# Kernel tuning notes

Measured on AMD Instinct MI355X. Metric: run time of the kernel, lower is better.

## Reference

```python
import jax, jax.numpy as jnp
import numpy as np

# Per-type input feature dims (NODE_DIM values); max dim = 128 = padded width of x.
NODE_DIMS = np.array([16, 32, 64, 128, 64, 32, 16, 128], dtype=np.int32)
N_TYPES = 8
MAX_DIM = 128
FEAT = 256          # node_feature_dim
N_GRAPHS = 100000   # batch_size; one node of each type per graph


def setup_inputs() -> dict:
    key = jax.random.key(0)
    k1, k2, k3 = jax.random.split(key, 3)
    num_nodes = N_GRAPHS * N_TYPES
    x = jax.random.normal(k1, (num_nodes, MAX_DIM), dtype=jnp.float32)
    # Per-type Linear weights, padded to MAX_DIM on the input axis.
    W = jax.random.normal(k2, (N_TYPES, FEAT, MAX_DIM), dtype=jnp.float32) * 0.05
    b = jax.random.normal(k3, (N_TYPES, FEAT), dtype=jnp.float32) * 0.05
    return {"x": x, "W": W, "b": b}


def reference(x, W, b):
    # Node n = g*N_TYPES + k is the type-k node of graph g (the gather index
    # ptr[b] + node_name.index(k) in the original). Dropout is eval-mode (identity).
    # Mask weight columns beyond each type's true input dim: equivalent to
    # slicing x[:, :NODE_DIM[k]] before the per-type Linear.
    mask = (jnp.arange(MAX_DIM)[None, None, :] < jnp.asarray(NODE_DIMS)[:, None, None]).astype(x.dtype)  # [T,1,D]
    W_eff = W * mask  # [T,F,D]
    xg = x.reshape(N_GRAPHS, N_TYPES, MAX_DIM)  # [G,T,D]
    y = jnp.einsum("gtd,tfd->gtf", xg, W_eff) + b[None, :, :]  # [G,T,F]
    return y.reshape(N_GRAPHS * N_TYPES, FEAT)
```

## Files before the change

### kernel.cpp

```cpp
#include <hip/hip_runtime.h>

#define N_GRAPHS 100000
#define NTYPES 8
#define MAXD 128
#define FEAT 256
#define ALDA 136
#define ELDA 68

typedef __attribute__((ext_vector_type(8))) short short8;
typedef __attribute__((ext_vector_type(4))) float f32x4;
typedef __attribute__((ext_vector_type(4))) unsigned uint4v;

constexpr int KSN[NTYPES]  = {1, 1, 2, 4, 2, 1, 1, 4};
constexpr int DIMS[NTYPES] = {16, 32, 64, 128, 64, 32, 16, 128};

__device__ __forceinline__ unsigned f2bf_u(float f) {
    unsigned u = __builtin_bit_cast(unsigned, f);
    return (u + 0x7fffu + ((u >> 16) & 1u)) >> 16;
}
__device__ __forceinline__ unsigned cvt2(float lo, float hi) {
    return f2bf_u(lo) | (f2bf_u(hi) << 16);
}
__device__ __forceinline__ short8 cvt8(f32x4 a, f32x4 b) {
    uint4v u;
    u.x = cvt2(a.x, a.y); u.y = cvt2(a.z, a.w);
    u.z = cvt2(b.x, b.y); u.w = cvt2(b.z, b.w);
    return __builtin_bit_cast(short8, u);
}

__global__ __launch_bounds__(256)
void prepack_w(const float* __restrict__ W, short8* __restrict__ wp)
{
    const int idx  = blockIdx.x * 256 + threadIdx.x;
    const int c16  = idx & 15;
    const int cgrp = (idx >> 4) & 3;
    const int ks   = (idx >> 6) & 3;
    const int ct   = (idx >> 8) & 15;
    const int t    = (idx >> 12) & 7;
    const int col  = ct * 16 + c16;
    const int k    = ks * 32 + cgrp * 8;
    const int dim  = 16 << ((0x30123210u >> (4 * t)) & 0xf);
    const float* src = W + ((size_t)t * FEAT + col) * MAXD + k;
    f32x4 a = *(const f32x4*)src;
    f32x4 b = *(const f32x4*)(src + 4);
    #pragma unroll
    for (int j = 0; j < 4; ++j) {
        if (k + j     >= dim) a[j] = 0.f;
        if (k + 4 + j >= dim) b[j] = 0.f;
    }
    wp[idx] = cvt8(a, b);
}

template<int T, bool PRE>
__device__ __forceinline__ void do_type(const float* __restrict__ x,
                                        const short8* __restrict__ wp,
                                        const float* __restrict__ W,
                                        const float* __restrict__ bias_g,
                                        float* __restrict__ out,
                                        unsigned short* __restrict__ as_,
                                        float* __restrict__ ep,
                                        int g0, int lane, int cgrp, int c16)
{
    constexpr int KS  = KSN[T];
    constexpr int NXT = (T + 1 < NTYPES) ? T + 1 : T;
    constexpr int KSn = KSN[NXT];
    constexpr int SPRn = KSn * 4;

    f32x4 pv[2 * KSn];
    if constexpr (T + 1 < NTYPES) {
        #pragma unroll
        for (int p = 0; p < KSn; ++p) {
            const int idx = p * 64 + lane;
            const int row = idx / SPRn, s8 = idx % SPRn;
            const float* rp = x + (((size_t)(g0 + row)) * NTYPES + (T + 1)) * MAXD + s8 * 8;
            pv[2 * p]     = __builtin_nontemporal_load((const f32x4*)rp);
            pv[2 * p + 1] = __builtin_nontemporal_load((const f32x4*)rp + 1);
        }
    }

    short8 a[KS];
    #pragma unroll
    for (int ks = 0; ks < KS; ++ks)
        a[ks] = *(const short8*)&as_[c16 * ALDA + ks * 32 + cgrp * 8];

    #pragma unroll
    for (int ct4 = 0; ct4 < 4; ++ct4) {
        #pragma unroll
        for (int c = 0; c < 4; ++c) {
            const int ct = ct4 * 4 + c;
            short8 wf[KS];
            if constexpr (PRE) {
                #pragma unroll
                for (int ks = 0; ks < KS; ++ks)
                    wf[ks] = wp[(((T * 16 + ct) * 4 + ks) * 4 + cgrp) * 16 + c16];
            } else {
                constexpr int DIM = DIMS[T];
                #pragma unroll
                for (int ks = 0; ks < KS; ++ks) {
                    const int k = ks * 32 + cgrp * 8;
                    const float* wfp = W + ((size_t)T * FEAT + ct * 16 + c16) * MAXD + k;
                    f32x4 wa = *(const f32x4*)wfp;
                    f32x4 wb = *(const f32x4*)(wfp + 4);
                    #pragma unroll
                    for (int j = 0; j < 4; ++j) {
                        if (k + j     >= DIM) wa[j] = 0.f;
                        if (k + 4 + j >= DIM) wb[j] = 0.f;
                    }
                    wf[ks] = cvt8(wa, wb);
                }
            }
            f32x4 acc = {0.f, 0.f, 0.f, 0.f};
            #pragma unroll
            for (int ks = 0; ks < KS; ++ks)
                acc = __builtin_amdgcn_mfma_f32_16x16x32_bf16(a[ks], wf[ks], acc, 0, 0, 0);
            #pragma unroll
            for (int r = 0; r < 4; ++r)
                ep[(cgrp * 4 + r) * ELDA + (ct & 3) * 16 + c16] = acc[r];
        }
        #pragma unroll
        for (int i = 0; i < 4; ++i) {
            const int row   = i * 4 + (lane >> 4);
            const int coldw = (lane & 15) * 4;
            f32x4 v  = *(const f32x4*)&ep[row * ELDA + coldw];
            f32x4 b4 = *(const f32x4*)&bias_g[T * FEAT + ct4 * 64 + coldw];
            f32x4 res;
            #pragma unroll
            for (int r = 0; r < 4; ++r) res[r] = v[r] + b4[r];
            __builtin_nontemporal_store(res,
                (f32x4*)&out[(((size_t)(g0 + row)) * NTYPES + T) * FEAT + ct4 * 64 + coldw]);
        }
    }

    if constexpr (T + 1 < NTYPES) {
        #pragma unroll
        for (int p = 0; p < KSn; ++p) {
            const int idx = p * 64 + lane;
            const int row = idx / SPRn, s8 = idx % SPRn;
            *(short8*)&as_[row * ALDA + s8 * 8] = cvt8(pv[2 * p], pv[2 * p + 1]);
        }
        do_type<T + 1, PRE>(x, wp, W, bias_g, out, as_, ep, g0, lane, cgrp, c16);
    }
}

template<bool PRE>
__global__ __launch_bounds__(256, 3)
void node_enc(const float* __restrict__ x, const short8* __restrict__ wp,
              const float* __restrict__ W, const float* __restrict__ bias_g,
              float* __restrict__ out)
{
    __shared__ __align__(16) unsigned short As[4][16 * ALDA];
    __shared__ __align__(16) float          Ep[4][16 * ELDA];
    const int tid  = threadIdx.x;
    const int lane = tid & 63;
    const int wave = tid >> 6;
    const int cgrp = lane >> 4;
    const int c16  = lane & 15;
    const int g0   = blockIdx.x * 64 + wave * 16;
    if (g0 >= N_GRAPHS) return;

    unsigned short* as_ = As[wave];
    {
        const int row = lane >> 2, s8 = lane & 3;
        const float* rp = x + (((size_t)(g0 + row)) * NTYPES + 0) * MAXD + s8 * 8;
        f32x4 v0 = __builtin_nontemporal_load((const f32x4*)rp);
        f32x4 v1 = __builtin_nontemporal_load((const f32x4*)rp + 1);
        *(short8*)&as_[row * ALDA + s8 * 8] = cvt8(v0, v1);
    }

    do_type<0, PRE>(x, wp, W, bias_g, out, as_, Ep[wave], g0, lane, cgrp, c16);
}

extern "C" void kernel_launch(void* const* d_in, const int* in_sizes, int n_in,
                              void* d_out, int out_size, void* d_ws, size_t ws_size,
                              hipStream_t stream)
{
    const float* x = (const float*)d_in[0];
    const float* W = (const float*)d_in[1];
    const float* b = (const float*)d_in[2];
    float* out = (float*)d_out;

    const int grid = (N_GRAPHS + 63) / 64;
    const size_t wp_bytes = (size_t)32768 * sizeof(short8);

    if (ws_size >= wp_bytes) {
        short8* wp = (short8*)d_ws;
        prepack_w<<<128, 256, 0, stream>>>(W, wp);
        node_enc<true><<<grid, 256, 0, stream>>>(x, wp, W, b, out);
    } else {
        node_enc<false><<<grid, 256, 0, stream>>>(x, nullptr, W, b, out);
    }
}
```

Baseline: 279.2 us.

## Merge A and epilogue LDS buffers, drop next-type prefetch, raise occupancy

Folds the bf16 A-tile buffer and the fp32 epilogue staging buffer into one per-wave LDS buffer, which shrinks shared memory per block. It removes the register prefetch of the next type's x rows, so those loads now happen after the current type's stores instead of overlapping with its compute. Launch bounds go from 3 to 8 blocks per CU so more waves can hide latency. The cost is losing explicit load/compute overlap and adding register-pressure limits. Safety relies on the next-type A writes coming after the epilogue reads of the same buffer within one wave.

```diff
diff --git a/kernel.cpp b/kernel.cpp
--- a/kernel.cpp
+++ b/kernel.cpp
@@ -4,8 +4,7 @@
 #define NTYPES 8
 #define MAXD 128
 #define FEAT 256
-#define ALDA 136
-#define ELDA 68
+#define LDR 68
 
 typedef __attribute__((ext_vector_type(8))) short short8;
 typedef __attribute__((ext_vector_type(4))) float f32x4;
@@ -21,11 +20,11 @@
 __device__ __forceinline__ unsigned cvt2(float lo, float hi) {
     return f2bf_u(lo) | (f2bf_u(hi) << 16);
 }
-__device__ __forceinline__ short8 cvt8(f32x4 a, f32x4 b) {
+__device__ __forceinline__ f32x4 cvt8f(f32x4 a, f32x4 b) {
     uint4v u;
     u.x = cvt2(a.x, a.y); u.y = cvt2(a.z, a.w);
     u.z = cvt2(b.x, b.y); u.w = cvt2(b.z, b.w);
-    return __builtin_bit_cast(short8, u);
+    return __builtin_bit_cast(f32x4, u);
 }
 
 __global__ __launch_bounds__(256)
@@ -48,7 +47,8 @@
         if (k + j     >= dim) a[j] = 0.f;
         if (k + 4 + j >= dim) b[j] = 0.f;
     }
-    wp[idx] = cvt8(a, b);
+    f32x4 r = cvt8f(a, b);
+    *(f32x4*)&wp[idx] = r;
 }
 
 template<int T, bool PRE>
@@ -57,31 +57,17 @@
                                         const float* __restrict__ W,
                                         const float* __restrict__ bias_g,
                                         float* __restrict__ out,
-                                        unsigned short* __restrict__ as_,
-                                        float* __restrict__ ep,
+                                        float* __restrict__ buf,
                                         int g0, int lane, int cgrp, int c16)
 {
-    constexpr int KS  = KSN[T];
-    constexpr int NXT = (T + 1 < NTYPES) ? T + 1 : T;
-    constexpr int KSn = KSN[NXT];
-    constexpr int SPRn = KSn * 4;
-
-    f32x4 pv[2 * KSn];
-    if constexpr (T + 1 < NTYPES) {
-        #pragma unroll
-        for (int p = 0; p < KSn; ++p) {
-            const int idx = p * 64 + lane;
-            const int row = idx / SPRn, s8 = idx % SPRn;
-            const float* rp = x + (((size_t)(g0 + row)) * NTYPES + (T + 1)) * MAXD + s8 * 8;
-            pv[2 * p]     = __builtin_nontemporal_load((const f32x4*)rp);
-            pv[2 * p + 1] = __builtin_nontemporal_load((const f32x4*)rp + 1);
-        }
-    }
+    constexpr int KS = KSN[T];
 
     short8 a[KS];
     #pragma unroll
-    for (int ks = 0; ks < KS; ++ks)
-        a[ks] = *(const short8*)&as_[c16 * ALDA + ks * 32 + cgrp * 8];
+    for (int ks = 0; ks < KS; ++ks) {
+        f32x4 tmp = *(const f32x4*)&buf[c16 * LDR + ks * 16 + cgrp * 4];
+        a[ks] = __builtin_bit_cast(short8, tmp);
+    }
 
     #pragma unroll
     for (int ct4 = 0; ct4 < 4; ++ct4) {
@@ -106,7 +92,7 @@
                         if (k + j     >= DIM) wa[j] = 0.f;
                         if (k + 4 + j >= DIM) wb[j] = 0.f;
                     }
-                    wf[ks] = cvt8(wa, wb);
+                    wf[ks] = __builtin_bit_cast(short8, cvt8f(wa, wb));
                 }
             }
             f32x4 acc = {0.f, 0.f, 0.f, 0.f};
@@ -115,13 +101,13 @@
                 acc = __builtin_amdgcn_mfma_f32_16x16x32_bf16(a[ks], wf[ks], acc, 0, 0, 0);
             #pragma unroll
             for (int r = 0; r < 4; ++r)
-                ep[(cgrp * 4 + r) * ELDA + (ct & 3) * 16 + c16] = acc[r];
+                buf[(cgrp * 4 + r) * LDR + c * 16 + c16] = acc[r];
         }
         #pragma unroll
         for (int i = 0; i < 4; ++i) {
             const int row   = i * 4 + (lane >> 4);
             const int coldw = (lane & 15) * 4;
-            f32x4 v  = *(const f32x4*)&ep[row * ELDA + coldw];
+            f32x4 v  = *(const f32x4*)&buf[row * LDR + coldw];
             f32x4 b4 = *(const f32x4*)&bias_g[T * FEAT + ct4 * 64 + coldw];
             f32x4 res;
             #pragma unroll
@@ -132,42 +118,47 @@
     }
 
     if constexpr (T + 1 < NTYPES) {
+        constexpr int KSn  = KSN[T + 1];
+        constexpr int SPRn = KSn * 4;
         #pragma unroll
         for (int p = 0; p < KSn; ++p) {
             const int idx = p * 64 + lane;
             const int row = idx / SPRn, s8 = idx % SPRn;
-            *(short8*)&as_[row * ALDA + s8 * 8] = cvt8(pv[2 * p], pv[2 * p + 1]);
+            const float* rp = x + (((size_t)(g0 + row)) * NTYPES + (T + 1)) * MAXD + s8 * 8;
+            f32x4 v0 = __builtin_nontemporal_load((const f32x4*)rp);
+            f32x4 v1 = __builtin_nontemporal_load((const f32x4*)rp + 1);
+            *(f32x4*)&buf[row * LDR + s8 * 4] = cvt8f(v0, v1);
         }
-        do_type<T + 1, PRE>(x, wp, W, bias_g, out, as_, ep, g0, lane, cgrp, c16);
+        do_type<T + 1, PRE>(x, wp, W, bias_g, out, buf, g0, lane, cgrp, c16);
     }
 }
 
 template<bool PRE>
-__global__ __launch_bounds__(256, 3)
+__global__ __launch_bounds__(256, 8)
 void node_enc(const float* __restrict__ x, const short8* __restrict__ wp,
               const float* __restrict__ W, const float* __restrict__ bias_g,
               float* __restrict__ out)
 {
-    __shared__ __align__(16) unsigned short As[4][16 * ALDA];
-    __shared__ __align__(16) float          Ep[4][16 * ELDA];
+    __shared__ __align__(16) float Buf[4][16 * LDR];
     const int tid  = threadIdx.x;
     const int lane = tid & 63;
     const int wave = tid >> 6;
     const int cgrp = lane >> 4;
     const int c16  = lane & 15;
-    const int g0   = blockIdx.x * 64 + wave * 16;
-    if (g0 >= N_GRAPHS) return;
+    const int w    = blockIdx.x * 4 + wave;
+    if (w >= N_GRAPHS / 16) return;
+    const int g0   = w * 16;
 
-    unsigned short* as_ = As[wave];
+    float* buf = Buf[wave];
     {
         const int row = lane >> 2, s8 = lane & 3;
         const float* rp = x + (((size_t)(g0 + row)) * NTYPES + 0) * MAXD + s8 * 8;
         f32x4 v0 = __builtin_nontemporal_load((const f32x4*)rp);
         f32x4 v1 = __builtin_nontemporal_load((const f32x4*)rp + 1);
-        *(short8*)&as_[row * ALDA + s8 * 8] = cvt8(v0, v1);
+        *(f32x4*)&buf[row * LDR + s8 * 4] = cvt8f(v0, v1);
     }
 
-    do_type<0, PRE>(x, wp, W, bias_g, out, as_, Ep[wave], g0, lane, cgrp, c16);
+    do_type<0, PRE>(x, wp, W, bias_g, out, buf, g0, lane, cgrp, c16);
 }
 
 extern "C" void kernel_launch(void* const* d_in, const int* in_sizes, int n_in,
@@ -179,7 +170,7 @@
     const float* b = (const float*)d_in[2];
     float* out = (float*)d_out;
 
-    const int grid = (N_GRAPHS + 63) / 64;
+    const int grid = (N_GRAPHS / 16 + 3) / 4;
     const size_t wp_bytes = (size_t)32768 * sizeof(short8);
 
     if (ws_size >= wp_bytes) {
```

After: 351.1 us. 25.8% more time.
